# Performance work log

Measured on AMD Instinct MI355X. Metric: run time of the kernel, lower is better.

Reference implementation:

```python
import jax, jax.numpy as jnp
import numpy as np

N, B, D, H, E = 1024, 8, 768, 8, 16384
DH = D // H
EPS = 1e-5


def setup_inputs() -> dict:
    key = jax.random.key(0)
    ks = jax.random.split(key, 12)
    s = 0.02
    return {
        "x": jax.random.normal(ks[0], (N, B, D), jnp.float32),
        "edge_index": jax.random.randint(ks[1], (B, 2, E), 0, N, jnp.int32),
        "gcn_W": jax.random.normal(ks[2], (D, D), jnp.float32) * s,
        "gcn_b": jnp.zeros((D,), jnp.float32),
        "in_proj_w": jax.random.normal(ks[3], (3 * D, D), jnp.float32) * s,
        "in_proj_b": jnp.zeros((3 * D,), jnp.float32),
        "out_proj_w": jax.random.normal(ks[4], (D, D), jnp.float32) * s,
        "out_proj_b": jnp.zeros((D,), jnp.float32),
        "gate_w": jax.random.normal(ks[5], (D, 2 * D), jnp.float32) * s,
        "gate_b": jnp.zeros((D,), jnp.float32),
        "ln_g": jnp.ones((D,), jnp.float32),
        "ln_b": jnp.zeros((D,), jnp.float32),
    }


def _gcn(xb, edge_index, gcn_W, gcn_b):
    # xb: [B, N, D] node features; edge_index: [B, 2, E]
    h = xb @ gcn_W.T  # linear first, as in PyG GCNConv
    loops = jnp.arange(N, dtype=edge_index.dtype)

    def agg(h_b, ei_b):
        src = jnp.concatenate([ei_b[0], loops])  # add self-loops
        dst = jnp.concatenate([ei_b[1], loops])
        deg = jax.ops.segment_sum(jnp.ones_like(src, h_b.dtype), dst, num_segments=N)
        dinv = jnp.where(deg > 0, jax.lax.rsqrt(deg), 0.0)
        norm = dinv[src] * dinv[dst]  # symmetric normalization
        msg = norm[:, None] * h_b[src]
        return jax.ops.segment_sum(msg, dst, num_segments=N)

    return jax.vmap(agg)(h, edge_index) + gcn_b  # [B, N, D]


def _mha(x, in_proj_w, in_proj_b, out_proj_w, out_proj_b):
    # x: [N, B, D] (seq-first, as nn.MultiheadAttention default)
    qkv = x @ in_proj_w.T + in_proj_b  # [N, B, 3D]
    q, k, v = jnp.split(qkv, 3, axis=-1)

    def heads(t):  # [N, B, D] -> [B, H, N, DH]
        return t.reshape(N, B, H, DH).transpose(1, 2, 0, 3)

    q, k, v = heads(q), heads(k), heads(v)
    scores = jnp.einsum("bhqd,bhkd->bhqk", q, k) / jnp.sqrt(jnp.float32(DH))
    attn = jax.nn.softmax(scores, axis=-1)
    ctx = jnp.einsum("bhqk,bhkd->bhqd", attn, v)  # [B, H, N, DH]
    ctx = ctx.transpose(2, 0, 1, 3).reshape(N, B, D)
    return ctx @ out_proj_w.T + out_proj_b


def _layernorm(x, g, b):
    mu = jnp.mean(x, axis=-1, keepdims=True)
    var = jnp.mean(jnp.square(x - mu), axis=-1, keepdims=True)
    return (x - mu) * jax.lax.rsqrt(var + EPS) * g + b


def reference(x, edge_index, gcn_W, gcn_b, in_proj_w, in_proj_b,
              out_proj_w, out_proj_b, gate_w, gate_b, ln_g, ln_b):
    xb = x.transpose(1, 0, 2)  # [B, N, D]
    gcn_out = _gcn(xb, edge_index, gcn_W, gcn_b).transpose(1, 0, 2)  # [N, B, D]
    attn_out = _mha(x, in_proj_w, in_proj_b, out_proj_w, out_proj_b)  # [N, B, D]
    combined = jnp.concatenate([gcn_out, attn_out], axis=-1)
    gate = jax.nn.sigmoid(combined @ gate_w.T + gate_b)
    fused = gate * gcn_out + (1.0 - gate) * attn_out
    return _layernorm(fused + x, ln_g, ln_b)
```

## Files before the change

### kernel.cpp

```cpp
#include <hip/hip_runtime.h>


typedef __attribute__((ext_vector_type(8))) short b16x8;
typedef __attribute__((ext_vector_type(4))) float f32x4;

using gu32 = __attribute__((address_space(1))) const unsigned int;
using lu32 = __attribute__((address_space(3))) unsigned int;

constexpr int N  = 1024;
constexpr int B  = 8;
constexpr int D  = 768;
constexpr int H  = 8;
constexpr int DH = 96;
constexpr int E  = 16384;
constexpr int M  = N * B;
constexpr float LN_EPS = 1e-5f;

#define DEV static __device__ __forceinline__
#define GLOAD(SRC, DST) __builtin_amdgcn_global_load_lds((gu32*)(SRC), (lu32*)(DST), 16, 0, 0)

DEV unsigned short f2b(float f) {
  unsigned u = __float_as_uint(f);
  u += 0x7fffu + ((u >> 16) & 1u);
  return (unsigned short)(u >> 16);
}
DEV float b2f(unsigned short h) { return __uint_as_float(((unsigned)h) << 16); }

constexpr int CS0 = 1572864;
constexpr int CS1 = CS0 + 147456;
constexpr int CS2 = CS1 + 442368;
constexpr int CS3 = CS2 + 147456;
constexpr int CS4 = CS3 + 294912;
__global__ void cast_all_kernel(
    const float* __restrict__ x, const float* __restrict__ gcnW,
    const float* __restrict__ ipw, const float* __restrict__ opw,
    const float* __restrict__ gw,
    unsigned short* __restrict__ xb16, unsigned short* __restrict__ wcat,
    unsigned short* __restrict__ wout, unsigned short* __restrict__ wgate) {
  const int i = blockIdx.x * 256 + threadIdx.x;
  if (i >= CS4) return;
  const float* in; unsigned short* out; int off;
  if (i < CS0)      { in = x;    out = xb16;           off = i; }
  else if (i < CS1) { in = gcnW; out = wcat;           off = i - CS0; }
  else if (i < CS2) { in = ipw;  out = wcat + 589824;  off = i - CS1; }
  else if (i < CS3) { in = opw;  out = wout;           off = i - CS2; }
  else              { in = gw;   out = wgate;          off = i - CS3; }
  float4 v = ((const float4*)in)[off];
  ushort4 o;
  o.x = f2b(v.x); o.y = f2b(v.y); o.z = f2b(v.z); o.w = f2b(v.w);
  ((ushort4*)out)[off] = o;
}

__global__ void zero_i32_kernel(int* __restrict__ p, int n) {
  int i = blockIdx.x * 256 + threadIdx.x;
  if (i < n) p[i] = 0;
}

__global__ void edge_count_kernel(const int* __restrict__ ei, int* __restrict__ cnt) {
  int i = blockIdx.x * 256 + threadIdx.x;
  int b = i >> 14, e = i & (E - 1);
  int dst = ei[(b << 15) + E + e];
  atomicAdd(&cnt[(b << 10) + dst], 1);
}

__global__ __launch_bounds__(1024) void scan_offs_kernel(
    const int* __restrict__ cnt, int* __restrict__ offs,
    int* __restrict__ cursor, float* __restrict__ dinv) {
  __shared__ int buf[1024];
  const int b = blockIdx.x, i = threadIdx.x, g = (b << 10) + i;
  const int c = cnt[g];
  buf[i] = c;
  __syncthreads();
  for (int off = 1; off < 1024; off <<= 1) {
    int t = (i >= off) ? buf[i - off] : 0;
    __syncthreads();
    buf[i] += t;
    __syncthreads();
  }
  const int excl = buf[i] - c;
  offs[g] = excl;
  cursor[g] = excl;
  dinv[g] = rsqrtf((float)(c + 1));
}

__global__ void edge_fill_kernel(const int* __restrict__ ei,
                                 int* __restrict__ cursor, int* __restrict__ elist) {
  int i = blockIdx.x * 256 + threadIdx.x;
  int b = i >> 14, e = i & (E - 1);
  int src = ei[(b << 15) + e];
  int dst = ei[(b << 15) + E + e];
  int slot = atomicAdd(&cursor[(b << 10) + dst], 1);
  elist[(b << 14) + slot] = src;
}

constexpr int EPI_FUSED = 0;
constexpr int EPI_ATTN  = 1;
constexpr int EPI_GATE  = 2;

template <int EPI, int BN, int K, int GX, int GY>
__global__ __launch_bounds__(256) void gemm_bt(
    const unsigned short* __restrict__ A, const unsigned short* __restrict__ W,
    const float* __restrict__ bias,
    void* __restrict__ p0, void* __restrict__ p1, void* __restrict__ p2,
    void* __restrict__ p3) {
  constexpr int NW = BN / 32;
  constexpr int NT = K / 32;
  __shared__ __align__(16) unsigned short sA[2][128][32];
  __shared__ __align__(16) unsigned short sB[2][BN][32];
  const int tid = threadIdx.x;
  const int lane = tid & 63, wid = tid >> 6;
  const int wm = wid >> 1, wn = wid & 1;
  const int bid = blockIdx.x;
  const int xcd = bid & 7, slot = bid >> 3;
  const int by = xcd * (GY / 8) + slot / GX;
  const int bx = slot % GX;
  const int m0 = by * 128, n0 = bx * BN;
  const int l15 = lane & 15, lhi = lane >> 4;
  const int srow = lane >> 2;
  const int scol = (((lane & 3) ^ ((lane >> 3) & 3))) * 8;
  const int rcol = ((lhi ^ ((l15 >> 1) & 3))) * 8;

  f32x4 acc[4][NW] = {};

  const unsigned short* pa = A + ((size_t)(m0 + wid * 32 + srow)) * K + scol;
  const unsigned short* pb = W + ((size_t)(n0 + wid * (BN / 4) + srow)) * K + scol;

  auto stage = [&](int buf) {
    GLOAD(pa,          &sA[buf][wid * 32][0]);
    GLOAD(pa + 16 * K, &sA[buf][wid * 32 + 16][0]);
    GLOAD(pb,          &sB[buf][wid * (BN / 4)][0]);
    if constexpr (BN == 128) GLOAD(pb + 16 * K, &sB[buf][wid * 32 + 16][0]);
    pa += 32; pb += 32;
  };

  stage(0);
  int cur = 0;
  for (int kt = 0; kt < NT; ++kt) {
    if (kt + 1 < NT) {
      stage(cur ^ 1);
      if constexpr (BN == 128) asm volatile("s_waitcnt vmcnt(4)" ::: "memory");
      else                     asm volatile("s_waitcnt vmcnt(3)" ::: "memory");
    } else {
      asm volatile("s_waitcnt vmcnt(0)" ::: "memory");
    }
    __builtin_amdgcn_s_barrier();
    __builtin_amdgcn_sched_barrier(0);

    b16x8 af[4], bfr[NW];
#pragma unroll
    for (int i = 0; i < 4; ++i)
      af[i] = *(const b16x8*)&sA[cur][wm * 64 + i * 16 + l15][rcol];
#pragma unroll
    for (int j = 0; j < NW; ++j)
      bfr[j] = *(const b16x8*)&sB[cur][wn * (BN / 2) + j * 16 + l15][rcol];
#pragma unroll
    for (int i = 0; i < 4; ++i)
#pragma unroll
      for (int j = 0; j < NW; ++j)
        acc[i][j] = __builtin_amdgcn_mfma_f32_16x16x32_bf16(af[i], bfr[j], acc[i][j], 0, 0, 0);

    __builtin_amdgcn_sched_barrier(0);
    __builtin_amdgcn_s_barrier();
    cur ^= 1;
  }

#pragma unroll
  for (int i = 0; i < 4; ++i) {
#pragma unroll
    for (int j = 0; j < NW; ++j) {
      const int c = n0 + wn * (BN / 2) + j * 16 + l15;
      float bv;
      if constexpr (EPI == EPI_FUSED) bv = (c < 768) ? 0.0f : bias[c - 768];
      else bv = bias[c];
#pragma unroll
      for (int g = 0; g < 4; ++g) {
        const int r = m0 + wm * 64 + i * 16 + lhi * 4 + g;
        float v = acc[i][j][g] + bv;
        if constexpr (EPI == EPI_FUSED) {
          const int n = r >> 3, b = r & 7;
          if (c < 768) {
            ((unsigned short*)p0)[((size_t)((b << 10) + n)) * 768 + c] = f2b(v);
          } else {
            const int cc2 = c - 768;
            const int sec = cc2 / 768, cc = cc2 - sec * 768;
            const int hd = cc / 96, dh = cc - hd * 96;
            unsigned short* dst =
                (sec == 0) ? (unsigned short*)p1
                           : (sec == 1 ? (unsigned short*)p2 : (unsigned short*)p3);
            size_t idx;
            if (sec < 2) idx = ((size_t)((b * 8 + hd) * 1024 + n)) * 96 + dh;
            else         idx = ((size_t)((b * 8 + hd) * 96 + dh)) * 1024 + n;
            dst[idx] = f2b(v);
          }
        } else if constexpr (EPI == EPI_ATTN) {
          ((unsigned short*)p0)[(size_t)r * 1536 + 768 + c] = f2b(v);
        } else {
          ((unsigned short*)p0)[(size_t)r * 768 + c] =
              f2b(1.0f / (1.0f + __expf(-v)));
        }
      }
    }
  }
}

__global__ __launch_bounds__(256) void attn_kernel(
    const unsigned short* __restrict__ qb, const unsigned short* __restrict__ kb,
    const unsigned short* __restrict__ vb, unsigned short* __restrict__ ctx) {
  __shared__ __align__(16) unsigned short sK[64][104];
  __shared__ __align__(16) unsigned short sV[96][72];
  __shared__ __align__(16) unsigned short sP[4][16][72];
  const int tid = threadIdx.x, lane = tid & 63, wid = tid >> 6;
  const int l15 = lane & 15, lhi = lane >> 4;
  const int bid = blockIdx.x;
  const int xcd = bid & 7, slot = bid >> 3;
  const int bh = xcd * 8 + (slot >> 4);
  const int q0 = (slot & 15) * 64;
  const float SCL = 0.14724445f;

  b16x8 qf[3];
  const size_t qbase = ((size_t)bh * 1024 + q0 + wid * 16 + l15) * 96 + lhi * 8;
#pragma unroll
  for (int ks = 0; ks < 3; ++ks) qf[ks] = *(const b16x8*)(qb + qbase + ks * 32);

  const int c0 = tid, c1 = 256 + tid, c2 = 512 + tid;
  const unsigned short* kp0 = kb + ((size_t)bh * 1024 + c0 / 12) * 96 + (c0 % 12) * 8;
  const unsigned short* kp1 = kb + ((size_t)bh * 1024 + c1 / 12) * 96 + (c1 % 12) * 8;
  const unsigned short* kp2 = kb + ((size_t)bh * 1024 + c2 / 12) * 96 + (c2 % 12) * 8;
  const unsigned short* vp0 = vb + ((size_t)bh * 96 + (c0 >> 3)) * 1024 + (c0 & 7) * 8;
  const unsigned short* vp1 = vb + ((size_t)bh * 96 + (c1 >> 3)) * 1024 + (c1 & 7) * 8;
  const unsigned short* vp2 = vb + ((size_t)bh * 96 + (c2 >> 3)) * 1024 + (c2 & 7) * 8;
  unsigned short* sk0 = &sK[c0 / 12][(c0 % 12) * 8];
  unsigned short* sk1 = &sK[c1 / 12][(c1 % 12) * 8];
  unsigned short* sk2 = &sK[c2 / 12][(c2 % 12) * 8];
  unsigned short* sv0 = &sV[c0 >> 3][(c0 & 7) * 8];
  unsigned short* sv1 = &sV[c1 >> 3][(c1 & 7) * 8];
  unsigned short* sv2 = &sV[c2 >> 3][(c2 & 7) * 8];

  uint4 k0 = *(const uint4*)kp0, k1 = *(const uint4*)kp1, k2 = *(const uint4*)kp2;
  uint4 v0 = *(const uint4*)vp0, v1 = *(const uint4*)vp1, v2 = *(const uint4*)vp2;

  f32x4 accO[6] = {};
  float ssum[4] = {0.f, 0.f, 0.f, 0.f};

  for (int kt = 0; kt < 16; ++kt) {
    __syncthreads();
    *(uint4*)sk0 = k0; *(uint4*)sk1 = k1; *(uint4*)sk2 = k2;
    *(uint4*)sv0 = v0; *(uint4*)sv1 = v1; *(uint4*)sv2 = v2;
    __syncthreads();
    if (kt < 15) {
      kp0 += 64 * 96; kp1 += 64 * 96; kp2 += 64 * 96;
      vp0 += 64;      vp1 += 64;      vp2 += 64;
      k0 = *(const uint4*)kp0; k1 = *(const uint4*)kp1; k2 = *(const uint4*)kp2;
      v0 = *(const uint4*)vp0; v1 = *(const uint4*)vp1; v2 = *(const uint4*)vp2;
    }

    f32x4 sf[4] = {};
#pragma unroll
    for (int f = 0; f < 4; ++f) {
#pragma unroll
      for (int ks = 0; ks < 3; ++ks) {
        b16x8 kf = *(const b16x8*)&sK[f * 16 + l15][ks * 32 + lhi * 8];
        sf[f] = __builtin_amdgcn_mfma_f32_16x16x32_bf16(qf[ks], kf, sf[f], 0, 0, 0);
      }
    }

#pragma unroll
    for (int g = 0; g < 4; ++g) {
#pragma unroll
      for (int f = 0; f < 4; ++f) {
        const float pv = exp2f(sf[f][g] * SCL);
        sP[wid][lhi * 4 + g][f * 16 + l15] = f2b(pv);
        ssum[g] += pv;
      }
    }

#pragma unroll
    for (int ks = 0; ks < 2; ++ks) {
      b16x8 pa = *(const b16x8*)&sP[wid][l15][ks * 32 + lhi * 8];
#pragma unroll
      for (int o = 0; o < 6; ++o) {
        b16x8 vf = *(const b16x8*)&sV[o * 16 + l15][ks * 32 + lhi * 8];
        accO[o] = __builtin_amdgcn_mfma_f32_16x16x32_bf16(pa, vf, accO[o], 0, 0, 0);
      }
    }
  }

#pragma unroll
  for (int g = 0; g < 4; ++g) {
#pragma unroll
    for (int msk = 1; msk < 16; msk <<= 1) ssum[g] += __shfl_xor(ssum[g], msk);
  }

  const int b = bh >> 3, hd = bh & 7;
  float rinv[4];
#pragma unroll
  for (int g = 0; g < 4; ++g) rinv[g] = 1.0f / ssum[g];
#pragma unroll
  for (int o = 0; o < 6; ++o)
#pragma unroll
    for (int g = 0; g < 4; ++g) {
      const int qrow = q0 + wid * 16 + lhi * 4 + g;
      ctx[((size_t)qrow * 8 + b) * 768 + hd * 96 + o * 16 + l15] =
          f2b(accO[o][g] * rinv[g]);
    }
}

__global__ __launch_bounds__(192) void gcn_agg_kernel(
    const unsigned short* __restrict__ h16,
    const int* __restrict__ cnt, const int* __restrict__ offs,
    const int* __restrict__ elist, const float* __restrict__ dinv,
    const float* __restrict__ gcn_b, unsigned short* __restrict__ cat16) {
  const int bn = blockIdx.x;
  const int b = bn >> 10, n = bn & 1023;
  const int d = threadIdx.x * 4;
  const float dn = dinv[bn];
  const size_t hrow = (size_t)bn * 768;
  ushort4 hv = *(const ushort4*)(h16 + hrow + d);
  float a0 = dn * dn * b2f(hv.x), a1 = dn * dn * b2f(hv.y);
  float a2 = dn * dn * b2f(hv.z), a3 = dn * dn * b2f(hv.w);
  const int st = offs[bn], cv = cnt[bn];
  const int* ep = elist + (b << 14) + st;
  int i = 0;
  for (; i + 2 <= cv; i += 2) {
    const int s0 = ep[i], s1 = ep[i + 1];
    const float nv0 = dinv[(b << 10) + s0] * dn;
    const float nv1 = dinv[(b << 10) + s1] * dn;
    const ushort4 r0 = *(const ushort4*)(h16 + ((size_t)((b << 10) + s0)) * 768 + d);
    const ushort4 r1 = *(const ushort4*)(h16 + ((size_t)((b << 10) + s1)) * 768 + d);
    a0 += nv0 * b2f(r0.x) + nv1 * b2f(r1.x);
    a1 += nv0 * b2f(r0.y) + nv1 * b2f(r1.y);
    a2 += nv0 * b2f(r0.z) + nv1 * b2f(r1.z);
    a3 += nv0 * b2f(r0.w) + nv1 * b2f(r1.w);
  }
  if (i < cv) {
    const int s0 = ep[i];
    const float nv0 = dinv[(b << 10) + s0] * dn;
    const ushort4 r0 = *(const ushort4*)(h16 + ((size_t)((b << 10) + s0)) * 768 + d);
    a0 += nv0 * b2f(r0.x); a1 += nv0 * b2f(r0.y);
    a2 += nv0 * b2f(r0.z); a3 += nv0 * b2f(r0.w);
  }
  const float4 bb = *(const float4*)(gcn_b + d);
  a0 += bb.x; a1 += bb.y; a2 += bb.z; a3 += bb.w;
  const size_t crow = ((size_t)n * 8 + b) * 1536;
  ushort4 co; co.x = f2b(a0); co.y = f2b(a1); co.z = f2b(a2); co.w = f2b(a3);
  *(ushort4*)(cat16 + crow + d) = co;
}

__global__ __launch_bounds__(192) void ln_fuse_kernel(
    const unsigned short* __restrict__ gate16,
    const unsigned short* __restrict__ cat16,
    const float* __restrict__ x,
    const float* __restrict__ lng, const float* __restrict__ lnb,
    float* __restrict__ out) {
  const int r = blockIdx.x;
  const int t = threadIdx.x, lane = t & 63, wid = t >> 6;
  const int d = t * 4;
  const size_t xrow = (size_t)r * 768;
  const size_t crow = (size_t)r * 1536;
  const ushort4 gv = *(const ushort4*)(gate16 + xrow + d);
  const ushort4 cv = *(const ushort4*)(cat16 + crow + d);
  const ushort4 av = *(const ushort4*)(cat16 + crow + 768 + d);
  const float4 xv = *(const float4*)(x + xrow + d);
  const float g0 = b2f(gv.x), g1 = b2f(gv.y), g2 = b2f(gv.z), g3 = b2f(gv.w);
  float f0 = g0 * b2f(cv.x) + (1.f - g0) * b2f(av.x) + xv.x;
  float f1 = g1 * b2f(cv.y) + (1.f - g1) * b2f(av.y) + xv.y;
  float f2 = g2 * b2f(cv.z) + (1.f - g2) * b2f(av.z) + xv.z;
  float f3 = g3 * b2f(cv.w) + (1.f - g3) * b2f(av.w) + xv.w;
  float s1 = f0 + f1 + f2 + f3;
  float s2 = f0 * f0 + f1 * f1 + f2 * f2 + f3 * f3;
#pragma unroll
  for (int msk = 1; msk < 64; msk <<= 1) {
    s1 += __shfl_xor(s1, msk);
    s2 += __shfl_xor(s2, msk);
  }
  __shared__ float p1[3], p2[3];
  if (lane == 0) { p1[wid] = s1; p2[wid] = s2; }
  __syncthreads();
  s1 = p1[0] + p1[1] + p1[2];
  s2 = p2[0] + p2[1] + p2[2];
  const float mu = s1 * (1.f / 768.f);
  float var = s2 * (1.f / 768.f) - mu * mu;
  var = fmaxf(var, 0.f);
  const float rstd = rsqrtf(var + LN_EPS);
  const float4 lg = *(const float4*)(lng + d);
  const float4 lb = *(const float4*)(lnb + d);
  float4 o;
  o.x = (f0 - mu) * rstd * lg.x + lb.x;
  o.y = (f1 - mu) * rstd * lg.y + lb.y;
  o.z = (f2 - mu) * rstd * lg.z + lb.z;
  o.w = (f3 - mu) * rstd * lg.w + lb.w;
  *(float4*)(out + xrow + d) = o;
}

extern "C" void kernel_launch(void* const* d_in, const int* in_sizes, int n_in,
                              void* d_out, int out_size, void* d_ws, size_t ws_size,
                              hipStream_t stream) {
  const float* x     = (const float*)d_in[0];
  const int*   ei    = (const int*)d_in[1];
  const float* gcnW  = (const float*)d_in[2];
  const float* gcnb  = (const float*)d_in[3];
  const float* ipw   = (const float*)d_in[4];
  const float* ipb   = (const float*)d_in[5];
  const float* opw   = (const float*)d_in[6];
  const float* opb   = (const float*)d_in[7];
  const float* gw    = (const float*)d_in[8];
  const float* gb    = (const float*)d_in[9];
  const float* lng   = (const float*)d_in[10];
  const float* lnb   = (const float*)d_in[11];
  float* out = (float*)d_out;

  char* p = (char*)d_ws;
  auto alloc = [&](size_t bytes) { void* q = p; p += (bytes + 255) & ~(size_t)255; return q; };

  unsigned short* xb16  = (unsigned short*)alloc((size_t)M * 768 * 2);
  unsigned short* wcat  = (unsigned short*)alloc((size_t)3072 * 768 * 2);
  unsigned short* wout  = (unsigned short*)alloc((size_t)768 * 768 * 2);
  unsigned short* wgate = (unsigned short*)alloc((size_t)768 * 1536 * 2);
  unsigned short* qb    = (unsigned short*)alloc((size_t)B * H * N * DH * 2);
  unsigned short* kb    = (unsigned short*)alloc((size_t)B * H * N * DH * 2);
  unsigned short* vb    = (unsigned short*)alloc((size_t)B * H * DH * N * 2);
  unsigned short* h16   = (unsigned short*)alloc((size_t)M * 768 * 2);
  unsigned short* cat16 = (unsigned short*)alloc((size_t)M * 1536 * 2);
  int* cnt    = (int*)alloc(8192 * 4);
  int* offs   = (int*)alloc(8192 * 4);
  int* cursor = (int*)alloc(8192 * 4);
  float* dinv = (float*)alloc(8192 * 4);
  int* elist  = (int*)alloc((size_t)B * E * 4);

  unsigned short* ctx16  = xb16;
  unsigned short* gate16 = qb;

  cast_all_kernel<<<(CS4 + 255) / 256, 256, 0, stream>>>(
      x, gcnW, ipw, opw, gw, xb16, wcat, wout, wgate);

  zero_i32_kernel<<<32, 256, 0, stream>>>(cnt, 8192);
  edge_count_kernel<<<(B * E) / 256, 256, 0, stream>>>(ei, cnt);
  scan_offs_kernel<<<8, 1024, 0, stream>>>(cnt, offs, cursor, dinv);
  edge_fill_kernel<<<(B * E) / 256, 256, 0, stream>>>(ei, cursor, elist);

  gemm_bt<EPI_FUSED, 128, 768, 24, 64><<<1536, 256, 0, stream>>>(
      xb16, wcat, ipb, (void*)h16, (void*)qb, (void*)kb, (void*)vb);
  attn_kernel<<<1024, 256, 0, stream>>>(qb, kb, vb, ctx16);
  gcn_agg_kernel<<<8192, 192, 0, stream>>>(h16, cnt, offs, elist, dinv, gcnb, cat16);
  gemm_bt<EPI_ATTN, 64, 768, 12, 64><<<768, 256, 0, stream>>>(
      ctx16, wout, opb, (void*)cat16, nullptr, nullptr, nullptr);
  gemm_bt<EPI_GATE, 64, 1536, 12, 64><<<768, 256, 0, stream>>>(
      cat16, wgate, gb, (void*)gate16, nullptr, nullptr, nullptr);

  ln_fuse_kernel<<<8192, 192, 0, stream>>>(gate16, cat16, x, lng, lnb, out);
}
```

Baseline: 257.7 us.

## Add 256x256-tile 8-wave GEMM for fused GCN/QKV projection

Replaces the fused GCN-linear plus QKV projection GEMM (M=8192, N=3072, K=768) with a dedicated kernel. It uses 256x256 output tiles, 512 threads and a 64-wide K step, and splits each step into four phases. In those phases the LDS fragment reads, async global-to-LDS loads for the next buffer, and MFMA bursts are interleaved with barriers and s_setprio. The larger tile raises reuse of operands loaded into LDS and cuts global traffic. The cost is a smaller grid (384 blocks), one block per CU, and heavy register pressure from 128 accumulator registers per thread.

Result: slower. 270.4 us (+4.9%).

```diff
diff --git a/kernel.cpp b/kernel.cpp
--- a/kernel.cpp
+++ b/kernel.cpp
@@ -93,16 +93,176 @@
   elist[(b << 14) + slot] = src;
 }
 
-constexpr int EPI_FUSED = 0;
-constexpr int EPI_ATTN  = 1;
-constexpr int EPI_GATE  = 2;
-
-template <int EPI, int BN, int K, int GX, int GY>
-__global__ __launch_bounds__(256) void gemm_bt(
+__global__ __launch_bounds__(512, 1) void gemm_fused256(
     const unsigned short* __restrict__ A, const unsigned short* __restrict__ W,
     const float* __restrict__ bias,
     void* __restrict__ p0, void* __restrict__ p1, void* __restrict__ p2,
     void* __restrict__ p3) {
+  constexpr int K = 768;
+  __shared__ __align__(16) unsigned short sA[2][2][256][32];
+  __shared__ __align__(16) unsigned short sB[2][2][256][32];
+  const int tid = threadIdx.x;
+  const int lane = tid & 63, wid = tid >> 6;
+  const int wm = wid >> 2, wn = wid & 3;
+  const int m0 = blockIdx.y * 256, n0 = blockIdx.x * 256;
+  const int l15 = lane & 15, lhi = lane >> 4;
+  const int rcol = (lhi ^ ((l15 >> 1) & 3)) * 8;
+  const int scol = (((tid & 3) ^ ((tid >> 3) & 3))) * 8;
+
+  f32x4 acc[8][4] = {};
+
+  const unsigned short* pa = A + ((size_t)(m0 + (tid >> 2))) * K + scol;
+  const unsigned short* pb = W + ((size_t)(n0 + (tid >> 2))) * K + scol;
+  constexpr size_t RS = (size_t)128 * K;
+
+  GLOAD(pb,           &sB[0][0][wid * 16][0]);
+  GLOAD(pb + RS,      &sB[0][0][128 + wid * 16][0]);
+  GLOAD(pa,           &sA[0][0][wid * 16][0]);
+  GLOAD(pa + RS,      &sA[0][0][128 + wid * 16][0]);
+  GLOAD(pb + 32,      &sB[0][1][wid * 16][0]);
+  GLOAD(pb + 32 + RS, &sB[0][1][128 + wid * 16][0]);
+  GLOAD(pa + 32,      &sA[0][1][wid * 16][0]);
+  GLOAD(pa + 32 + RS, &sA[0][1][128 + wid * 16][0]);
+  asm volatile("s_waitcnt vmcnt(4)" ::: "memory");
+  __builtin_amdgcn_s_barrier();
+
+  for (int t = 0; t < 12; ++t) {
+    const int p = t & 1;
+    const bool stg = (t < 11);
+    const int kn = (t + 1) * 64;
+    b16x8 af[4], bf[4];
+
+#pragma unroll
+    for (int cf = 0; cf < 4; ++cf)
+      bf[cf] = *(const b16x8*)&sB[p][0][wn * 64 + cf * 16 + l15][rcol];
+#pragma unroll
+    for (int rf = 0; rf < 4; ++rf)
+      af[rf] = *(const b16x8*)&sA[p][0][wm * 128 + rf * 16 + l15][rcol];
+    if (stg) {
+      GLOAD(pb + kn,      &sB[p ^ 1][0][wid * 16][0]);
+      GLOAD(pb + kn + RS, &sB[p ^ 1][0][128 + wid * 16][0]);
+    }
+    __builtin_amdgcn_sched_barrier(0);
+    __builtin_amdgcn_s_barrier();
+    asm volatile("s_waitcnt lgkmcnt(0)" ::: "memory");
+    __builtin_amdgcn_sched_barrier(0);
+    __builtin_amdgcn_s_setprio(1);
+#pragma unroll
+    for (int rf = 0; rf < 4; ++rf)
+#pragma unroll
+      for (int cf = 0; cf < 4; ++cf)
+        acc[rf][cf] = __builtin_amdgcn_mfma_f32_16x16x32_bf16(af[rf], bf[cf], acc[rf][cf], 0, 0, 0);
+    __builtin_amdgcn_s_setprio(0);
+    __builtin_amdgcn_sched_barrier(0);
+    __builtin_amdgcn_s_barrier();
+
+#pragma unroll
+    for (int rf = 0; rf < 4; ++rf)
+      af[rf] = *(const b16x8*)&sA[p][0][wm * 128 + 64 + rf * 16 + l15][rcol];
+    if (stg) {
+      GLOAD(pa + kn,      &sA[p ^ 1][0][wid * 16][0]);
+      GLOAD(pa + kn + RS, &sA[p ^ 1][0][128 + wid * 16][0]);
+    }
+    __builtin_amdgcn_sched_barrier(0);
+    if (stg) asm volatile("s_waitcnt vmcnt(4)" ::: "memory");
+    else     asm volatile("s_waitcnt vmcnt(0)" ::: "memory");
+    __builtin_amdgcn_s_barrier();
+    asm volatile("s_waitcnt lgkmcnt(0)" ::: "memory");
+    __builtin_amdgcn_sched_barrier(0);
+    __builtin_amdgcn_s_setprio(1);
+#pragma unroll
+    for (int rf = 0; rf < 4; ++rf)
+#pragma unroll
+      for (int cf = 0; cf < 4; ++cf)
+        acc[4 + rf][cf] = __builtin_amdgcn_mfma_f32_16x16x32_bf16(af[rf], bf[cf], acc[4 + rf][cf], 0, 0, 0);
+    __builtin_amdgcn_s_setprio(0);
+    __builtin_amdgcn_sched_barrier(0);
+    __builtin_amdgcn_s_barrier();
+
+#pragma unroll
+    for (int cf = 0; cf < 4; ++cf)
+      bf[cf] = *(const b16x8*)&sB[p][1][wn * 64 + cf * 16 + l15][rcol];
+#pragma unroll
+    for (int rf = 0; rf < 4; ++rf)
+      af[rf] = *(const b16x8*)&sA[p][1][wm * 128 + rf * 16 + l15][rcol];
+    if (stg) {
+      GLOAD(pb + kn + 32,      &sB[p ^ 1][1][wid * 16][0]);
+      GLOAD(pb + kn + 32 + RS, &sB[p ^ 1][1][128 + wid * 16][0]);
+    }
+    __builtin_amdgcn_sched_barrier(0);
+    __builtin_amdgcn_s_barrier();
+    asm volatile("s_waitcnt lgkmcnt(0)" ::: "memory");
+    __builtin_amdgcn_sched_barrier(0);
+    __builtin_amdgcn_s_setprio(1);
+#pragma unroll
+    for (int rf = 0; rf < 4; ++rf)
+#pragma unroll
+      for (int cf = 0; cf < 4; ++cf)
+        acc[rf][cf] = __builtin_amdgcn_mfma_f32_16x16x32_bf16(af[rf], bf[cf], acc[rf][cf], 0, 0, 0);
+    __builtin_amdgcn_s_setprio(0);
+    __builtin_amdgcn_sched_barrier(0);
+    __builtin_amdgcn_s_barrier();
+
+#pragma unroll
+    for (int rf = 0; rf < 4; ++rf)
+      af[rf] = *(const b16x8*)&sA[p][1][wm * 128 + 64 + rf * 16 + l15][rcol];
+    if (stg) {
+      GLOAD(pa + kn + 32,      &sA[p ^ 1][1][wid * 16][0]);
+      GLOAD(pa + kn + 32 + RS, &sA[p ^ 1][1][128 + wid * 16][0]);
+    }
+    __builtin_amdgcn_sched_barrier(0);
+    if (stg) asm volatile("s_waitcnt vmcnt(4)" ::: "memory");
+    __builtin_amdgcn_s_barrier();
+    asm volatile("s_waitcnt lgkmcnt(0)" ::: "memory");
+    __builtin_amdgcn_sched_barrier(0);
+    __builtin_amdgcn_s_setprio(1);
+#pragma unroll
+    for (int rf = 0; rf < 4; ++rf)
+#pragma unroll
+      for (int cf = 0; cf < 4; ++cf)
+        acc[4 + rf][cf] = __builtin_amdgcn_mfma_f32_16x16x32_bf16(af[rf], bf[cf], acc[4 + rf][cf], 0, 0, 0);
+    __builtin_amdgcn_s_setprio(0);
+    __builtin_amdgcn_sched_barrier(0);
+    __builtin_amdgcn_s_barrier();
+  }
+
+#pragma unroll
+  for (int rg = 0; rg < 8; ++rg) {
+#pragma unroll
+    for (int cf = 0; cf < 4; ++cf) {
+      const int c = n0 + wn * 64 + cf * 16 + l15;
+      const float bv = (c < 768) ? 0.0f : bias[c - 768];
+#pragma unroll
+      for (int g = 0; g < 4; ++g) {
+        const int r = m0 + wm * 128 + rg * 16 + lhi * 4 + g;
+        float v = acc[rg][cf][g] + bv;
+        const int n = r >> 3, b = r & 7;
+        if (c < 768) {
+          ((unsigned short*)p0)[((size_t)((b << 10) + n)) * 768 + c] = f2b(v);
+        } else {
+          const int cc2 = c - 768;
+          const int sec = cc2 / 768, cc = cc2 - sec * 768;
+          const int hd = cc / 96, dh = cc - hd * 96;
+          unsigned short* dst =
+              (sec == 0) ? (unsigned short*)p1
+                         : (sec == 1 ? (unsigned short*)p2 : (unsigned short*)p3);
+          size_t idx;
+          if (sec < 2) idx = ((size_t)((b * 8 + hd) * 1024 + n)) * 96 + dh;
+          else         idx = ((size_t)((b * 8 + hd) * 96 + dh)) * 1024 + n;
+          dst[idx] = f2b(v);
+        }
+      }
+    }
+  }
+}
+
+constexpr int EPI_ATTN  = 1;
+constexpr int EPI_GATE  = 2;
+
+template <int EPI, int BN, int K, int GX, int GY>
+__global__ __launch_bounds__(256) void gemm_bt(
+    const unsigned short* __restrict__ A, const unsigned short* __restrict__ W,
+    const float* __restrict__ bias, void* __restrict__ p0) {
   constexpr int NW = BN / 32;
   constexpr int NT = K / 32;
   __shared__ __align__(16) unsigned short sA[2][128][32];
@@ -169,30 +329,12 @@
 #pragma unroll
     for (int j = 0; j < NW; ++j) {
       const int c = n0 + wn * (BN / 2) + j * 16 + l15;
-      float bv;
-      if constexpr (EPI == EPI_FUSED) bv = (c < 768) ? 0.0f : bias[c - 768];
-      else bv = bias[c];
+      const float bv = bias[c];
 #pragma unroll
       for (int g = 0; g < 4; ++g) {
         const int r = m0 + wm * 64 + i * 16 + lhi * 4 + g;
         float v = acc[i][j][g] + bv;
-        if constexpr (EPI == EPI_FUSED) {
-          const int n = r >> 3, b = r & 7;
-          if (c < 768) {
-            ((unsigned short*)p0)[((size_t)((b << 10) + n)) * 768 + c] = f2b(v);
-          } else {
-            const int cc2 = c - 768;
-            const int sec = cc2 / 768, cc = cc2 - sec * 768;
-            const int hd = cc / 96, dh = cc - hd * 96;
-            unsigned short* dst =
-                (sec == 0) ? (unsigned short*)p1
-                           : (sec == 1 ? (unsigned short*)p2 : (unsigned short*)p3);
-            size_t idx;
-            if (sec < 2) idx = ((size_t)((b * 8 + hd) * 1024 + n)) * 96 + dh;
-            else         idx = ((size_t)((b * 8 + hd) * 96 + dh)) * 1024 + n;
-            dst[idx] = f2b(v);
-          }
-        } else if constexpr (EPI == EPI_ATTN) {
+        if constexpr (EPI == EPI_ATTN) {
           ((unsigned short*)p0)[(size_t)r * 1536 + 768 + c] = f2b(v);
         } else {
           ((unsigned short*)p0)[(size_t)r * 768 + c] =
@@ -438,14 +580,14 @@
   scan_offs_kernel<<<8, 1024, 0, stream>>>(cnt, offs, cursor, dinv);
   edge_fill_kernel<<<(B * E) / 256, 256, 0, stream>>>(ei, cursor, elist);
 
-  gemm_bt<EPI_FUSED, 128, 768, 24, 64><<<1536, 256, 0, stream>>>(
+  gemm_fused256<<<dim3(12, 32), 512, 0, stream>>>(
       xb16, wcat, ipb, (void*)h16, (void*)qb, (void*)kb, (void*)vb);
   attn_kernel<<<1024, 256, 0, stream>>>(qb, kb, vb, ctx16);
   gcn_agg_kernel<<<8192, 192, 0, stream>>>(h16, cnt, offs, elist, dinv, gcnb, cat16);
   gemm_bt<EPI_ATTN, 64, 768, 12, 64><<<768, 256, 0, stream>>>(
-      ctx16, wout, opb, (void*)cat16, nullptr, nullptr, nullptr);
+      ctx16, wout, opb, (void*)cat16);
   gemm_bt<EPI_GATE, 64, 1536, 12, 64><<<768, 256, 0, stream>>>(
-      cat16, wgate, gb, (void*)gate16, nullptr, nullptr, nullptr);
+      cat16, wgate, gb, (void*)gate16);
 
   ln_fuse_kernel<<<8192, 192, 0, stream>>>(gate16, cat16, x, lng, lnb, out);
 }
```
